# Kernel optimization log

Hardware: AMD Instinct MI355X
Metric: run time of the kernel (lower is better)

The kernel has to match this reference:

```python
import jax, jax.numpy as jnp
import numpy as np

T, V, D = 8, 100000, 128   # tables, rows per table, embedding dim
B = 4096                   # batch (bags per table)
N = 204800                 # total jagged values per table (avg pooling factor 50)


def setup_inputs() -> dict:
    key = jax.random.key(0)
    k1, k2, k3, k4 = jax.random.split(key, 4)
    tables = jax.random.normal(k1, (T, V, D), dtype=jnp.float32) * 0.01
    values = jax.random.randint(k2, (T, N), 0, V, dtype=jnp.int32)
    # offsets per table: [0, sorted interior points, N]  (include_last_offset=True)
    interior = jnp.sort(jax.random.randint(k3, (T, B - 1), 0, N, dtype=jnp.int32), axis=1)
    zeros = jnp.zeros((T, 1), dtype=jnp.int32)
    ends = jnp.full((T, 1), N, dtype=jnp.int32)
    offsets = jnp.concatenate([zeros, interior, ends], axis=1)  # [T, B+1]
    per_sample_weights = jax.random.uniform(k4, (T, N), dtype=jnp.float32)
    return {"tables": tables, "values": values, "offsets": offsets,
            "per_sample_weights": per_sample_weights}


def reference(tables, values, offsets, per_sample_weights):
    # One EmbeddingBag(mode='sum', include_last_offset=True) per table, vmapped.
    n = values.shape[1]

    def one_table(w, vals, offs, psw):
        emb = w[vals] * psw[:, None]                      # [N, D] weighted gather
        # segment id of position i: j s.t. offs[j] <= i < offs[j+1]
        seg = jnp.searchsorted(offs, jnp.arange(n, dtype=offs.dtype), side='right') - 1
        return jax.ops.segment_sum(emb, seg, num_segments=B)  # [B, D]

    pooled = jax.vmap(one_table)(tables, values, offsets, per_sample_weights)  # [T, B, D]
    # concat per-table pooled embeddings along feature dim -> [B, T*D]
    return jnp.transpose(pooled, (1, 0, 2)).reshape(B, T * D)
```

## Files before the change

kernel.cpp:

```cpp
#include <hip/hip_runtime.h>
#include <hip/hip_bf16.h>


namespace {
constexpr int T = 8;
constexpr int V = 100000;
constexpr int D = 128;
constexpr int B = 4096;
constexpr int N = 204800;
}

__global__ __launch_bounds__(128) void grouped_ebag_kernel(
    const float* __restrict__ tables,
    const int* __restrict__ values,
    const int* __restrict__ offsets,
    const float* __restrict__ psw,
    float* __restrict__ out)
{
    const int bag = blockIdx.x;
    const int t = bag >> 12;
    const int b = bag & (B - 1);
    const int d = threadIdx.x;

    const int start = offsets[t * (B + 1) + b];
    const int end   = offsets[t * (B + 1) + b + 1];

    const float* __restrict__ tab  = tables + (size_t)t * V * D;
    const int*   __restrict__ vals = values + (size_t)t * N;
    const float* __restrict__ w    = psw    + (size_t)t * N;

    float acc0 = 0.0f;
    float acc1 = 0.0f;

    int i = start;
    for (; i + 1 < end; i += 2) {
        const int   v0 = vals[i];
        const int   v1 = vals[i + 1];
        const float w0 = w[i];
        const float w1 = w[i + 1];
        const float e0 = tab[(size_t)v0 * D + d];
        const float e1 = tab[(size_t)v1 * D + d];
        acc0 = fmaf(e0, w0, acc0);
        acc1 = fmaf(e1, w1, acc1);
    }
    if (i < end) {
        const int   v0 = vals[i];
        const float w0 = w[i];
        acc0 = fmaf(tab[(size_t)v0 * D + d], w0, acc0);
    }

    out[(size_t)b * (T * D) + t * D + d] = acc0 + acc1;
}

extern "C" void kernel_launch(void* const* d_in, const int* in_sizes, int n_in,
                              void* d_out, int out_size, void* d_ws, size_t ws_size,
                              hipStream_t stream) {
    const float* tables  = (const float*)d_in[0];
    const int*   values  = (const int*)d_in[1];
    const int*   offsets = (const int*)d_in[2];
    const float* psw     = (const float*)d_in[3];
    float*       out     = (float*)d_out;

    dim3 grid(T * B);
    dim3 block(D);
    grouped_ebag_kernel<<<grid, block, 0, stream>>>(tables, values, offsets, psw, out);
}
```

Measured before the change: 656.6 us.

## Map one wavefront per bag with float4 row loads and prefetched indices

Each 64-lane wavefront now handles one bag. Each half-wave gathers alternating rows with float4 vector loads, and the two halves are combined with a cross-lane shuffle at the end. The next group of indices and weights is prefetched ahead of the gathers to hide index-load latency, and each block of 256 threads now holds four bags. This widens the memory transactions and raises the number of rows in flight per wave, at the cost of more registers and a more complex tail path.

Measured after the change: 572.1 us. 1.15x faster.

```diff
diff --git a/kernel.cpp b/kernel.cpp
--- a/kernel.cpp
+++ b/kernel.cpp
@@ -10,46 +10,95 @@
 constexpr int N = 204800;
 }
 
-__global__ __launch_bounds__(128) void grouped_ebag_kernel(
+__global__ __launch_bounds__(256) void grouped_ebag_kernel(
     const float* __restrict__ tables,
     const int* __restrict__ values,
     const int* __restrict__ offsets,
     const float* __restrict__ psw,
     float* __restrict__ out)
 {
-    const int bag = blockIdx.x;
+    const int wave = threadIdx.x >> 6;
+    const int lane = threadIdx.x & 63;
+    const int bag  = (blockIdx.x << 2) + wave;
     const int t = bag >> 12;
     const int b = bag & (B - 1);
-    const int d = threadIdx.x;
+    const int half = lane >> 5;
+    const int c4   = lane & 31;
 
     const int start = offsets[t * (B + 1) + b];
     const int end   = offsets[t * (B + 1) + b + 1];
 
-    const float* __restrict__ tab  = tables + (size_t)t * V * D;
+    const float* __restrict__ tab  = tables + (size_t)t * (V * D);
     const int*   __restrict__ vals = values + (size_t)t * N;
-    const float* __restrict__ w    = psw    + (size_t)t * N;
+    const float* __restrict__ wgt  = psw    + (size_t)t * N;
 
-    float acc0 = 0.0f;
-    float acc1 = 0.0f;
+    float4 acc = make_float4(0.f, 0.f, 0.f, 0.f);
+
+    const int len  = end - start;
+    const int ngrp = len >> 3;
+
+    int   v[4];
+    float wv[4];
+    if (ngrp > 0) {
+#pragma unroll
+        for (int j = 0; j < 4; ++j) {
+            v[j]  = vals[start + 2 * j + half];
+            wv[j] = wgt [start + 2 * j + half];
+        }
+    }
 
     int i = start;
-    for (; i + 1 < end; i += 2) {
-        const int   v0 = vals[i];
-        const int   v1 = vals[i + 1];
-        const float w0 = w[i];
-        const float w1 = w[i + 1];
-        const float e0 = tab[(size_t)v0 * D + d];
-        const float e1 = tab[(size_t)v1 * D + d];
-        acc0 = fmaf(e0, w0, acc0);
-        acc1 = fmaf(e1, w1, acc1);
-    }
-    if (i < end) {
-        const int   v0 = vals[i];
-        const float w0 = w[i];
-        acc0 = fmaf(tab[(size_t)v0 * D + d], w0, acc0);
+    for (int g = 0; g < ngrp; ++g) {
+        int   vn[4] = {0, 0, 0, 0};
+        float wn[4] = {0.f, 0.f, 0.f, 0.f};
+        const int inext = i + 8;
+        if (g + 1 < ngrp) {
+#pragma unroll
+            for (int j = 0; j < 4; ++j) {
+                vn[j] = vals[inext + 2 * j + half];
+                wn[j] = wgt [inext + 2 * j + half];
+            }
+        }
+#pragma unroll
+        for (int j = 0; j < 4; ++j) {
+            const float4 e = *(const float4*)(tab + (size_t)v[j] * D + c4 * 4);
+            acc.x = fmaf(e.x, wv[j], acc.x);
+            acc.y = fmaf(e.y, wv[j], acc.y);
+            acc.z = fmaf(e.z, wv[j], acc.z);
+            acc.w = fmaf(e.w, wv[j], acc.w);
+        }
+#pragma unroll
+        for (int j = 0; j < 4; ++j) { v[j] = vn[j]; wv[j] = wn[j]; }
+        i = inext;
     }
 
-    out[(size_t)b * (T * D) + t * D + d] = acc0 + acc1;
+    for (; i + 2 <= end; i += 2) {
+        const int   vv = vals[i + half];
+        const float ww = wgt [i + half];
+        const float4 e = *(const float4*)(tab + (size_t)vv * D + c4 * 4);
+        acc.x = fmaf(e.x, ww, acc.x);
+        acc.y = fmaf(e.y, ww, acc.y);
+        acc.z = fmaf(e.z, ww, acc.z);
+        acc.w = fmaf(e.w, ww, acc.w);
+    }
+    if (i < end && half == 0) {
+        const int   vv = vals[i];
+        const float ww = wgt [i];
+        const float4 e = *(const float4*)(tab + (size_t)vv * D + c4 * 4);
+        acc.x = fmaf(e.x, ww, acc.x);
+        acc.y = fmaf(e.y, ww, acc.y);
+        acc.z = fmaf(e.z, ww, acc.z);
+        acc.w = fmaf(e.w, ww, acc.w);
+    }
+
+    acc.x += __shfl_xor(acc.x, 32);
+    acc.y += __shfl_xor(acc.y, 32);
+    acc.z += __shfl_xor(acc.z, 32);
+    acc.w += __shfl_xor(acc.w, 32);
+
+    if (half == 0) {
+        *(float4*)(out + (size_t)b * (T * D) + t * D + c4 * 4) = acc;
+    }
 }
 
 extern "C" void kernel_launch(void* const* d_in, const int* in_sizes, int n_in,
@@ -61,7 +110,7 @@
     const float* psw     = (const float*)d_in[3];
     float*       out     = (float*)d_out;
 
-    dim3 grid(T * B);
-    dim3 block(D);
+    dim3 grid((T * B) / 4);
+    dim3 block(256);
     grouped_ebag_kernel<<<grid, block, 0, stream>>>(tables, values, offsets, psw, out);
 }
```

## Map one wave per bag with float2 loads and double-buffered gather groups

Applied to the files above, without the earlier changes.

Each 64-lane wavefront now handles one bag, with each lane loading a float2 so one wave covers the 128-wide row. Four bags are packed into each 256-thread block. The bag's indices are processed in groups of eight gathers, double-buffered so the next group's row loads are in flight while the current group is accumulated. The aim is more memory-level parallelism on the random row gathers and fewer blocks. The cost is higher register use, and short bags fall back to a scalar tail loop.

Measured after the change: 587.3 us. 10.6% less time.

```diff
diff --git a/kernel.cpp b/kernel.cpp
--- a/kernel.cpp
+++ b/kernel.cpp
@@ -10,46 +10,79 @@
 constexpr int N = 204800;
 }
 
-__global__ __launch_bounds__(128) void grouped_ebag_kernel(
+__global__ __launch_bounds__(256) void grouped_ebag_kernel(
     const float* __restrict__ tables,
     const int* __restrict__ values,
     const int* __restrict__ offsets,
     const float* __restrict__ psw,
     float* __restrict__ out)
 {
-    const int bag = blockIdx.x;
+    const int wave = threadIdx.x >> 6;
+    const int lane = threadIdx.x & 63;
+    const int bag  = (blockIdx.x << 2) + wave;
     const int t = bag >> 12;
     const int b = bag & (B - 1);
-    const int d = threadIdx.x;
 
     const int start = offsets[t * (B + 1) + b];
     const int end   = offsets[t * (B + 1) + b + 1];
+    const int len   = end - start;
 
-    const float* __restrict__ tab  = tables + (size_t)t * V * D;
-    const int*   __restrict__ vals = values + (size_t)t * N;
-    const float* __restrict__ w    = psw    + (size_t)t * N;
+    const float2* __restrict__ tab2 = (const float2*)(tables + (size_t)t * (V * D));
+    const int*    __restrict__ vals = values + (size_t)t * N;
+    const float*  __restrict__ wgt  = psw    + (size_t)t * N;
 
-    float acc0 = 0.0f;
-    float acc1 = 0.0f;
+    float2 acc = make_float2(0.f, 0.f);
 
-    int i = start;
-    for (; i + 1 < end; i += 2) {
-        const int   v0 = vals[i];
-        const int   v1 = vals[i + 1];
-        const float w0 = w[i];
-        const float w1 = w[i + 1];
-        const float e0 = tab[(size_t)v0 * D + d];
-        const float e1 = tab[(size_t)v1 * D + d];
-        acc0 = fmaf(e0, w0, acc0);
-        acc1 = fmaf(e1, w1, acc1);
-    }
-    if (i < end) {
-        const int   v0 = vals[i];
-        const float w0 = w[i];
-        acc0 = fmaf(tab[(size_t)v0 * D + d], w0, acc0);
+    auto load_group = [&](int ii, float* w, float2* d) {
+        int v[8];
+#pragma unroll
+        for (int j = 0; j < 8; ++j) {
+            v[j] = vals[ii + j];
+            w[j] = wgt [ii + j];
+        }
+#pragma unroll
+        for (int j = 0; j < 8; ++j) {
+            d[j] = tab2[(v[j] << 6) + lane];
+        }
+    };
+    auto consume = [&](const float* w, const float2* d) {
+#pragma unroll
+        for (int j = 0; j < 8; ++j) {
+            acc.x = fmaf(d[j].x, w[j], acc.x);
+            acc.y = fmaf(d[j].y, w[j], acc.y);
+        }
+    };
+
+    const int ngrp = len >> 3;
+    if (ngrp >= 1) {
+        float wA[8]; float2 dA[8];
+        float wB[8]; float2 dB[8];
+        load_group(start, wA, dA);
+        int g = 1;
+        for (; g + 1 < ngrp; g += 2) {
+            load_group(start + (g << 3), wB, dB);
+            consume(wA, dA);
+            load_group(start + ((g + 1) << 3), wA, dA);
+            consume(wB, dB);
+        }
+        if (g < ngrp) {
+            load_group(start + (g << 3), wB, dB);
+            consume(wA, dA);
+            consume(wB, dB);
+        } else {
+            consume(wA, dA);
+        }
     }
 
-    out[(size_t)b * (T * D) + t * D + d] = acc0 + acc1;
+    for (int i = start + (ngrp << 3); i < end; ++i) {
+        const int   v = vals[i];
+        const float w = wgt[i];
+        const float2 e = tab2[(v << 6) + lane];
+        acc.x = fmaf(e.x, w, acc.x);
+        acc.y = fmaf(e.y, w, acc.y);
+    }
+
+    *(float2*)(out + (size_t)b * (T * D) + t * D + lane * 2) = acc;
 }
 
 extern "C" void kernel_launch(void* const* d_in, const int* in_sizes, int n_in,
@@ -61,7 +94,7 @@
     const float* psw     = (const float*)d_in[3];
     float*       out     = (float*)d_out;
 
-    dim3 grid(T * B);
-    dim3 block(D);
+    dim3 grid((T * B) / 4);
+    dim3 block(256);
     grouped_ebag_kernel<<<grid, block, 0, stream>>>(tables, values, offsets, psw, out);
 }
```
